# Performance work log

Measured on AMD Instinct MI355X. Metric: run time of the kernel, lower is better.

## Reference

```python
import jax, jax.numpy as jnp
import numpy as np

N_NODES = 100000
D_IN = 128
H_DIM = 128
N_EDGES = 1600000


def _gcn_conv(x, src, dst, dinv, W, b):
    # PyG GCNConv(improved=True): h = x @ W; out = A_hat h + b,
    # A_hat = D^{-1/2} (A + 2I) D^{-1/2}
    h = x @ W                                   # [N, H]
    norm = dinv[src] * dinv[dst]                # [E]
    agg = jnp.zeros_like(h).at[dst].add(h[src] * norm[:, None])
    agg = agg + h * (2.0 * dinv * dinv)[:, None]  # self-loop, weight 2.0
    return agg + b


def setup_inputs() -> dict:
    key = jax.random.key(0)
    ks = jax.random.split(key, 12)
    s = 1.0 / np.sqrt(D_IN)
    sh = 1.0 / np.sqrt(2 * H_DIM)
    inp = {
        "x": jax.random.normal(ks[0], (N_NODES, D_IN), jnp.float32),
        "edge_index": jax.random.randint(ks[1], (2, N_EDGES), 0, N_NODES, jnp.int64),
        # GCNConv weights (in -> hidden), bias
        "Wz": jax.random.uniform(ks[2], (D_IN, H_DIM), jnp.float32, -s, s),
        "bz": jnp.zeros((H_DIM,), jnp.float32),
        "Wr": jax.random.uniform(ks[3], (D_IN, H_DIM), jnp.float32, -s, s),
        "br": jnp.zeros((H_DIM,), jnp.float32),
        "Wh": jax.random.uniform(ks[4], (D_IN, H_DIM), jnp.float32, -s, s),
        "bh": jnp.zeros((H_DIM,), jnp.float32),
        # TGCN gate linears: Linear(2h, h)
        "lzW": jax.random.uniform(ks[5], (2 * H_DIM, H_DIM), jnp.float32, -sh, sh),
        "lzb": jax.random.uniform(ks[6], (H_DIM,), jnp.float32, -sh, sh),
        "lrW": jax.random.uniform(ks[7], (2 * H_DIM, H_DIM), jnp.float32, -sh, sh),
        "lrb": jax.random.uniform(ks[8], (H_DIM,), jnp.float32, -sh, sh),
        "lhW": jax.random.uniform(ks[9], (2 * H_DIM, H_DIM), jnp.float32, -sh, sh),
        "lhb": jax.random.uniform(ks[10], (H_DIM,), jnp.float32, -sh, sh),
        # final linear2: hidden -> 1
        "W2": jax.random.uniform(ks[11], (H_DIM, 1), jnp.float32, -1 / np.sqrt(H_DIM), 1 / np.sqrt(H_DIM)),
        "b2": jnp.zeros((1,), jnp.float32),
    }
    return inp


def reference(x, edge_index, Wz, bz, Wr, br, Wh, bh, lzW, lzb, lrW, lrb, lhW, lhb, W2, b2):
    src, dst = edge_index[0], edge_index[1]
    n = x.shape[0]
    # improved GCN norm: deg includes self-loop weight 2
    deg = jnp.zeros((n,), x.dtype).at[dst].add(jnp.ones_like(src, x.dtype)) + 2.0
    dinv = jnp.where(deg > 0, deg ** -0.5, 0.0)
    # TGCN cell with H0 = 0
    H0 = jnp.zeros((n, Wz.shape[1]), x.dtype)
    Z = jax.nn.sigmoid(jnp.concatenate([_gcn_conv(x, src, dst, dinv, Wz, bz), H0], axis=1) @ lzW + lzb)
    R = jax.nn.sigmoid(jnp.concatenate([_gcn_conv(x, src, dst, dinv, Wr, br), H0], axis=1) @ lrW + lrb)
    Ht = jnp.tanh(jnp.concatenate([_gcn_conv(x, src, dst, dinv, Wh, bh), H0 * R], axis=1) @ lhW + lhb)
    H = Z * H0 + (1.0 - Z) * Ht
    # forward: relu output is discarded (y = h overwrites), then linear2
    return H @ W2 + b2
```

## Files before the change

### kernel.cpp

```cpp
#include <hip/hip_runtime.h>
#include <math.h>

#define D 128
#define BSHIFT 9
#define NB 196
#define EPT 7
#define P1B 241
#define CAPB 80
#define PSTRIDE (P1B * CAPB)
#define ECAP 9216
#define XCB2 3125
#define PRB 32

typedef __attribute__((ext_vector_type(8))) short s8v;
typedef __attribute__((ext_vector_type(8))) unsigned short us8;
typedef __attribute__((ext_vector_type(4))) unsigned short us4;
typedef __attribute__((ext_vector_type(4))) float f4v;

__device__ __forceinline__ float bf2f(unsigned short u) {
    union { unsigned int i; float f; } v; v.i = ((unsigned int)u) << 16; return v.f;
}
__device__ __forceinline__ unsigned short f2bf(float f) {
    union { float f; unsigned int i; } v; v.f = f;
    unsigned int r = v.i + 0x7FFFu + ((v.i >> 16) & 1u);
    return (unsigned short)(r >> 16);
}

__global__ __launch_bounds__(1024) void k_pre(
    const int* __restrict__ src, const int* __restrict__ dst, int E,
    unsigned int* __restrict__ pairs, int* __restrict__ runlen,
    const float* __restrict__ x, unsigned short* __restrict__ xb, int n4,
    const float* __restrict__ Wz, const float* __restrict__ bz,
    const float* __restrict__ lzW, const float* __restrict__ lzb,
    const float* __restrict__ Wh, const float* __restrict__ bh,
    const float* __restrict__ lhW, const float* __restrict__ lhb,
    unsigned short* __restrict__ Mt, float* __restrict__ c) {
    __shared__ int cnt[256];
    __shared__ int loff[256];
    __shared__ unsigned int stage[EPT * 1024];
    int bx = blockIdx.x, tid = threadIdx.x;

    if (bx < P1B) {
        unsigned int pk[EPT]; int rkbk[EPT];
        int e0 = bx * (EPT * 1024) + tid;
        if (tid < 256) cnt[tid] = 0;
        __syncthreads();
        #pragma unroll
        for (int i = 0; i < EPT; ++i) {
            int e = e0 + i * 1024;
            bool ok = e < E;
            int d = ok ? dst[e] : 0;
            int s = ok ? src[e] : 0;
            int bk = d >> BSHIFT;
            pk[i] = ((unsigned int)(d & ((1 << BSHIFT) - 1)) << 17) | (unsigned int)s;
            int r = ok ? atomicAdd(&cnt[bk], 1) : 0;
            rkbk[i] = ok ? ((bk << 16) | r) : -1;
        }
        __syncthreads();
        if (tid < 64) {
            int v0 = cnt[tid * 4], v1 = cnt[tid * 4 + 1], v2 = cnt[tid * 4 + 2], v3 = cnt[tid * 4 + 3];
            int s = v0 + v1 + v2 + v3;
            int sc = s;
            #pragma unroll
            for (int off = 1; off < 64; off <<= 1) {
                int o = __shfl_up(sc, off, 64);
                if (tid >= off) sc += o;
            }
            int excl = sc - s;
            loff[tid * 4]     = excl;
            loff[tid * 4 + 1] = excl + v0;
            loff[tid * 4 + 2] = excl + v0 + v1;
            loff[tid * 4 + 3] = excl + v0 + v1 + v2;
        }
        __syncthreads();
        #pragma unroll
        for (int i = 0; i < EPT; ++i) {
            if (rkbk[i] >= 0) {
                int bk = rkbk[i] >> 16;
                stage[loff[bk] + (rkbk[i] & 0xffff)] = pk[i];
            }
        }
        if (tid < 256) runlen[bx * 256 + tid] = cnt[tid];
        __syncthreads();
        int wv = tid >> 6, lane = tid & 63;
        for (int b = wv; b < 256; b += 16) {
            int len = cnt[b];
            if (len == 0) continue;
            int lo = loff[b];
            unsigned int gbase = (unsigned int)b * PSTRIDE + (unsigned int)bx * CAPB;
            for (int j = lane; j < len; j += 64)
                pairs[gbase + j] = stage[lo + j];
        }
    } else if (bx < P1B + XCB2) {
        int i = (bx - P1B) * 1024 + tid;
        if (i < n4) {
            float4 v = ((const float4*)x)[i];
            us4 o;
            o[0] = f2bf(v.x); o[1] = f2bf(v.y); o[2] = f2bf(v.z); o[3] = f2bf(v.w);
            ((us4*)xb)[i] = o;
        }
    } else {
        int k = (bx - (P1B + XCB2)) * 4 + (tid >> 8);
        int j = tid & 255;
        int jj = j & 127;
        const float* W = (j < 128) ? Wz : Wh;
        const float* L = (j < 128) ? lzW : lhW;
        float s = 0.f;
        for (int t = 0; t < 128; ++t) s += W[k * 128 + t] * L[t * 128 + jj];
        Mt[(size_t)j * 128 + k] = f2bf(s);
        if (k == 0) {
            const float* b  = (j < 128) ? bz  : bh;
            const float* lb = (j < 128) ? lzb : lhb;
            float cs = lb[jj];
            for (int t = 0; t < 128; ++t) cs += b[t] * L[t * 128 + jj];
            c[j] = cs;
        }
    }
}

__global__ __launch_bounds__(1024) void k_part2(
    const unsigned int* __restrict__ pairs, const int* __restrict__ runlen,
    int N,
    int* __restrict__ rowptr, int* __restrict__ deg, float* __restrict__ dinv,
    int* __restrict__ esrc) {
    __shared__ int cnt2[512];
    __shared__ int lcur[512];
    __shared__ int rl[256];
    __shared__ int sstage[ECAP];
    __shared__ int stot;
    int b = blockIdx.x, tid = threadIdx.x;
    int n0 = b << BSHIFT;
    int nn = min(N - n0, 1 << BSHIFT);
    long pb = (long)b * PSTRIDE;
    int wv = tid >> 6, lane = tid & 63;

    if (tid < 256) rl[tid] = (tid < P1B) ? runlen[tid * 256 + b] : 0;
    if (tid < 512) cnt2[tid] = 0;
    __syncthreads();
    for (int r = wv; r < P1B; r += 16) {
        int len = rl[r];
        long rb = pb + r * CAPB;
        for (int j = lane; j < len; j += 64)
            atomicAdd(&cnt2[pairs[rb + j] >> 17], 1);
    }
    __syncthreads();
    if (tid < 64) {
        int v[8]; int s = 0;
        #pragma unroll
        for (int k = 0; k < 8; ++k) { v[k] = cnt2[tid * 8 + k]; s += v[k]; }
        int sc = s;
        #pragma unroll
        for (int off = 1; off < 64; off <<= 1) {
            int o = __shfl_up(sc, off, 64);
            if (tid >= off) sc += o;
        }
        int excl = sc - s;
        if (tid == 63) stot = sc;
        #pragma unroll
        for (int k = 0; k < 8; ++k) {
            int node = tid * 8 + k;
            lcur[node] = excl;
            if (node < nn) {
                rowptr[n0 + node] = b * ECAP + excl;
                deg[n0 + node]    = v[k];
                dinv[n0 + node]   = rsqrtf((float)v[k] + 2.0f);
            }
            excl += v[k];
        }
    }
    __syncthreads();
    for (int r = wv; r < P1B; r += 16) {
        int len = rl[r];
        long rb = pb + r * CAPB;
        for (int j = lane; j < len; j += 64) {
            unsigned int p = pairs[rb + j];
            int pos = atomicAdd(&lcur[p >> 17], 1);
            sstage[pos] = (int)(p & 0x1FFFFu);
        }
    }
    __syncthreads();
    int tot = stot;
    for (int i = tid; i < tot; i += 1024)
        esrc[b * ECAP + i] = sstage[i];
}

#define ASTRIDE 136
__global__ __launch_bounds__(512, 6) void k_gep(
    const unsigned short* __restrict__ xb,
    const int* __restrict__ esrc, const int* __restrict__ rowptr,
    const int* __restrict__ deg, const float* __restrict__ dinv,
    const unsigned short* __restrict__ Mt, const float* __restrict__ c,
    const float* __restrict__ W2, const float* __restrict__ b2,
    float* __restrict__ out, int N) {
    __shared__ unsigned short Ast[32 * ASTRIDE];
    __shared__ float pbuf[8][32];

    int tid = threadIdx.x;
    int n0 = blockIdx.x * 32;
    int grp = tid >> 4, sub = tid & 15;
    int node = n0 + grp;
    bool valid = node < N;

    int start = 0, dcnt = 0;
    float dd = 0.f;
    us8 xs = {0, 0, 0, 0, 0, 0, 0, 0};
    if (valid) {
        start = rowptr[node];
        dcnt  = deg[node];
        dd    = dinv[node];
        xs = *(const us8*)(xb + (size_t)node * D + sub * 8);
    }
    float acc[8];
    #pragma unroll
    for (int j = 0; j < 8; ++j) acc[j] = 0.f;

    for (int base = 0; base < dcnt; base += 16) {
        int cnt = min(16, dcnt - base);
        int myedge = 0; float mynorm = 0.f;
        if (sub < cnt) { myedge = esrc[start + base + sub]; mynorm = dinv[myedge]; }
        int i = 0;
        for (; i + 3 < cnt; i += 4) {
            int   s0 = __shfl(myedge, i,     16); float w0 = __shfl(mynorm, i,     16);
            int   s1 = __shfl(myedge, i + 1, 16); float w1 = __shfl(mynorm, i + 1, 16);
            int   s2 = __shfl(myedge, i + 2, 16); float w2 = __shfl(mynorm, i + 2, 16);
            int   s3 = __shfl(myedge, i + 3, 16); float w3 = __shfl(mynorm, i + 3, 16);
            us8 v0 = *(const us8*)(xb + (size_t)s0 * D + sub * 8);
            us8 v1 = *(const us8*)(xb + (size_t)s1 * D + sub * 8);
            us8 v2 = *(const us8*)(xb + (size_t)s2 * D + sub * 8);
            us8 v3 = *(const us8*)(xb + (size_t)s3 * D + sub * 8);
            #pragma unroll
            for (int j = 0; j < 8; ++j) acc[j] += bf2f(v0[j]) * w0;
            #pragma unroll
            for (int j = 0; j < 8; ++j) acc[j] += bf2f(v1[j]) * w1;
            #pragma unroll
            for (int j = 0; j < 8; ++j) acc[j] += bf2f(v2[j]) * w2;
            #pragma unroll
            for (int j = 0; j < 8; ++j) acc[j] += bf2f(v3[j]) * w3;
        }
        for (; i < cnt; ++i) {
            int   s0 = __shfl(myedge, i, 16); float w0 = __shfl(mynorm, i, 16);
            us8 v0 = *(const us8*)(xb + (size_t)s0 * D + sub * 8);
            #pragma unroll
            for (int j = 0; j < 8; ++j) acc[j] += bf2f(v0[j]) * w0;
        }
    }
    {
        float sfac = 2.f * dd * dd;
        us8 r;
        #pragma unroll
        for (int j = 0; j < 8; ++j) r[j] = f2bf(acc[j] * dd + bf2f(xs[j]) * sfac);
        *(us8*)&Ast[grp * ASTRIDE + sub * 8] = r;
    }
    __syncthreads();

    int wv = tid >> 6;
    int lane = tid & 63;
    int l = lane & 15, q = lane >> 4;

    f4v acc2[2][2];
    #pragma unroll
    for (int zi = 0; zi < 2; ++zi)
        #pragma unroll
        for (int nt = 0; nt < 2; ++nt) acc2[zi][nt] = (f4v){0.f, 0.f, 0.f, 0.f};

    const unsigned short* Bb = Mt + (size_t)l * 128 + q * 8;

    #pragma unroll
    for (int ks = 0; ks < 4; ++ks) {
        s8v bz_ = *(const s8v*)(Bb + (size_t)wv * 16 * 128 + ks * 32);
        s8v bh_ = *(const s8v*)(Bb + (size_t)(8 + wv) * 16 * 128 + ks * 32);
        #pragma unroll
        for (int nt = 0; nt < 2; ++nt) {
            s8v a = *(const s8v*)&Ast[(nt * 16 + l) * ASTRIDE + ks * 32 + q * 8];
            acc2[0][nt] = __builtin_amdgcn_mfma_f32_16x16x32_bf16(a, bz_, acc2[0][nt], 0, 0, 0);
            acc2[1][nt] = __builtin_amdgcn_mfma_f32_16x16x32_bf16(a, bh_, acc2[1][nt], 0, 0, 0);
        }
    }

    {
        int col = wv * 16 + l;
        float cz = c[col], ch = c[128 + col], w2 = W2[col];
        float p[2][4];
        #pragma unroll
        for (int nt = 0; nt < 2; ++nt)
            #pragma unroll
            for (int r = 0; r < 4; ++r) {
                float gz = acc2[0][nt][r] + cz;
                float gh = acc2[1][nt][r] + ch;
                float z  = 1.f / (1.f + __expf(-gz));
                float ht = 1.f - 2.f / (__expf(2.f * gh) + 1.f);
                p[nt][r] = (1.f - z) * ht * w2;
            }
        #pragma unroll
        for (int nt = 0; nt < 2; ++nt)
            #pragma unroll
            for (int r = 0; r < 4; ++r) {
                p[nt][r] += __shfl_xor(p[nt][r], 1);
                p[nt][r] += __shfl_xor(p[nt][r], 2);
                p[nt][r] += __shfl_xor(p[nt][r], 4);
                p[nt][r] += __shfl_xor(p[nt][r], 8);
            }
        if (l == 0) {
            #pragma unroll
            for (int nt = 0; nt < 2; ++nt)
                #pragma unroll
                for (int r = 0; r < 4; ++r)
                    pbuf[wv][nt * 16 + q * 4 + r] = p[nt][r];
        }
    }
    __syncthreads();
    if (tid < 32) {
        int n = n0 + tid;
        if (n < N) {
            float s = b2[0];
            #pragma unroll
            for (int cp = 0; cp < 8; ++cp) s += pbuf[cp][tid];
            out[n] = s;
        }
    }
}

extern "C" void kernel_launch(void* const* d_in, const int* in_sizes, int n_in,
                              void* d_out, int out_size, void* d_ws, size_t ws_size,
                              hipStream_t stream) {
    const float* x    = (const float*)d_in[0];
    const int*   eidx = (const int*)d_in[1];
    const float* Wz   = (const float*)d_in[2];
    const float* bz   = (const float*)d_in[3];
    const float* Wh   = (const float*)d_in[6];
    const float* bh   = (const float*)d_in[7];
    const float* lzW  = (const float*)d_in[8];
    const float* lzb  = (const float*)d_in[9];
    const float* lhW  = (const float*)d_in[12];
    const float* lhb  = (const float*)d_in[13];
    const float* W2   = (const float*)d_in[14];
    const float* b2   = (const float*)d_in[15];
    float* out = (float*)d_out;

    int N = in_sizes[0] / D;
    int E = in_sizes[1] / 2;
    const int* src = eidx;
    const int* dst = eidx + E;

    char* ws = (char*)d_ws;
    size_t off = 0;
    auto alloc = [&](size_t bytes) { void* p = ws + off; off += (bytes + 511) & ~(size_t)511; return p; };
    unsigned short* xb  = (unsigned short*)alloc((size_t)N * D * 2);
    unsigned int*   pairs = (unsigned int*)alloc((size_t)NB * PSTRIDE * 4);
    int*   rowptr = (int*)  alloc((size_t)N * 4);
    int*   deg    = (int*)  alloc((size_t)N * 4);
    float* dinv   = (float*)alloc((size_t)N * 4);
    int*   esrc   = (int*)  alloc((size_t)NB * ECAP * 4);
    int*   runlen = (int*)  alloc((size_t)P1B * 256 * 4);
    unsigned short* Mt = (unsigned short*)alloc(256 * 128 * 2);
    float* c      = (float*)alloc(256 * 4);

    int n4 = N * (D / 4);
    k_pre<<<P1B + XCB2 + PRB, 1024, 0, stream>>>(
        src, dst, E, pairs, runlen,
        x, xb, n4, Wz, bz, lzW, lzb, Wh, bh, lhW, lhb, Mt, c);
    k_part2<<<NB, 1024, 0, stream>>>(pairs, runlen, N, rowptr, deg, dinv, esrc);
    k_gep<<<(N + 31) / 32, 512, 0, stream>>>(
        xb, esrc, rowptr, deg, dinv, Mt, c, W2, b2, out, N);
}
```

Before: 231.2 us.

## Process 64 nodes per gather block with split-edge half-warps and coarsen bf16 cast

The gather-GEMM kernel now handles 64 nodes per block. Each 32-lane group processes four node rows in sequence, and its two 16-lane halves take alternating edges, then combine partial sums with a shuffle-xor. The MFMA stage now covers four 16-row tiles per wave, so each loaded B fragment from Mt is reused across more rows. The x-to-bf16 conversion blocks each process four float4 chunks per thread, giving fewer blocks. This aims to amortize per-block overhead and Mt loads and to raise memory-level parallelism in the gather. The cost is fewer blocks, more LDS use and higher register pressure.

```diff
diff --git a/kernel.cpp b/kernel.cpp
--- a/kernel.cpp
+++ b/kernel.cpp
@@ -9,7 +9,7 @@
 #define CAPB 80
 #define PSTRIDE (P1B * CAPB)
 #define ECAP 9216
-#define XCB2 3125
+#define XCB4 782
 #define PRB 32
 
 typedef __attribute__((ext_vector_type(8))) short s8v;
@@ -91,16 +91,20 @@
             for (int j = lane; j < len; j += 64)
                 pairs[gbase + j] = stage[lo + j];
         }
-    } else if (bx < P1B + XCB2) {
-        int i = (bx - P1B) * 1024 + tid;
-        if (i < n4) {
-            float4 v = ((const float4*)x)[i];
-            us4 o;
-            o[0] = f2bf(v.x); o[1] = f2bf(v.y); o[2] = f2bf(v.z); o[3] = f2bf(v.w);
-            ((us4*)xb)[i] = o;
+    } else if (bx < P1B + XCB4) {
+        int i0 = (bx - P1B) * 4096 + tid;
+        #pragma unroll
+        for (int u = 0; u < 4; ++u) {
+            int i = i0 + u * 1024;
+            if (i < n4) {
+                float4 v = ((const float4*)x)[i];
+                us4 o;
+                o[0] = f2bf(v.x); o[1] = f2bf(v.y); o[2] = f2bf(v.z); o[3] = f2bf(v.w);
+                ((us4*)xb)[i] = o;
+            }
         }
     } else {
-        int k = (bx - (P1B + XCB2)) * 4 + (tid >> 8);
+        int k = (bx - (P1B + XCB4)) * 4 + (tid >> 8);
         int j = tid & 255;
         int jj = j & 127;
         const float* W = (j < 128) ? Wz : Wh;
@@ -192,64 +196,74 @@
     const unsigned short* __restrict__ Mt, const float* __restrict__ c,
     const float* __restrict__ W2, const float* __restrict__ b2,
     float* __restrict__ out, int N) {
-    __shared__ unsigned short Ast[32 * ASTRIDE];
-    __shared__ float pbuf[8][32];
+    __shared__ unsigned short Ast[64 * ASTRIDE];
+    __shared__ float pbuf[8][64];
 
     int tid = threadIdx.x;
-    int n0 = blockIdx.x * 32;
-    int grp = tid >> 4, sub = tid & 15;
-    int node = n0 + grp;
-    bool valid = node < N;
-
-    int start = 0, dcnt = 0;
-    float dd = 0.f;
-    us8 xs = {0, 0, 0, 0, 0, 0, 0, 0};
-    if (valid) {
-        start = rowptr[node];
-        dcnt  = deg[node];
-        dd    = dinv[node];
-        xs = *(const us8*)(xb + (size_t)node * D + sub * 8);
-    }
-    float acc[8];
-    #pragma unroll
-    for (int j = 0; j < 8; ++j) acc[j] = 0.f;
-
-    for (int base = 0; base < dcnt; base += 16) {
-        int cnt = min(16, dcnt - base);
-        int myedge = 0; float mynorm = 0.f;
-        if (sub < cnt) { myedge = esrc[start + base + sub]; mynorm = dinv[myedge]; }
-        int i = 0;
-        for (; i + 3 < cnt; i += 4) {
-            int   s0 = __shfl(myedge, i,     16); float w0 = __shfl(mynorm, i,     16);
-            int   s1 = __shfl(myedge, i + 1, 16); float w1 = __shfl(mynorm, i + 1, 16);
-            int   s2 = __shfl(myedge, i + 2, 16); float w2 = __shfl(mynorm, i + 2, 16);
-            int   s3 = __shfl(myedge, i + 3, 16); float w3 = __shfl(mynorm, i + 3, 16);
-            us8 v0 = *(const us8*)(xb + (size_t)s0 * D + sub * 8);
-            us8 v1 = *(const us8*)(xb + (size_t)s1 * D + sub * 8);
-            us8 v2 = *(const us8*)(xb + (size_t)s2 * D + sub * 8);
-            us8 v3 = *(const us8*)(xb + (size_t)s3 * D + sub * 8);
-            #pragma unroll
-            for (int j = 0; j < 8; ++j) acc[j] += bf2f(v0[j]) * w0;
-            #pragma unroll
-            for (int j = 0; j < 8; ++j) acc[j] += bf2f(v1[j]) * w1;
-            #pragma unroll
-            for (int j = 0; j < 8; ++j) acc[j] += bf2f(v2[j]) * w2;
-            #pragma unroll
-            for (int j = 0; j < 8; ++j) acc[j] += bf2f(v3[j]) * w3;
-        }
-        for (; i < cnt; ++i) {
-            int   s0 = __shfl(myedge, i, 16); float w0 = __shfl(mynorm, i, 16);
-            us8 v0 = *(const us8*)(xb + (size_t)s0 * D + sub * 8);
-            #pragma unroll
-            for (int j = 0; j < 8; ++j) acc[j] += bf2f(v0[j]) * w0;
-        }
-    }
-    {
-        float sfac = 2.f * dd * dd;
-        us8 r;
-        #pragma unroll
-        for (int j = 0; j < 8; ++j) r[j] = f2bf(acc[j] * dd + bf2f(xs[j]) * sfac);
-        *(us8*)&Ast[grp * ASTRIDE + sub * 8] = r;
+    int n0 = blockIdx.x * 64;
+    int hw = tid >> 5, sub = tid & 31;
+    int eo = sub >> 4, cs = sub & 15;
+
+    for (int t = 0; t < 4; ++t) {
+        int row = t * 16 + hw;
+        int node = n0 + row;
+        bool valid = node < N;
+        int start = 0, dcnt = 0;
+        float dd = 0.f;
+        us8 xs = {0, 0, 0, 0, 0, 0, 0, 0};
+        if (valid) {
+            start = rowptr[node];
+            dcnt  = deg[node];
+            dd    = dinv[node];
+            if (eo == 0) xs = *(const us8*)(xb + (size_t)node * D + cs * 8);
+        }
+        float acc[8];
+        #pragma unroll
+        for (int j = 0; j < 8; ++j) acc[j] = 0.f;
+
+        int end = start + dcnt;
+        for (int base = start; base < end; base += 32) {
+            int cnt = min(32, end - base);
+            int myedge = 0; float mynorm = 0.f;
+            if (sub < cnt) { myedge = esrc[base + sub]; mynorm = dinv[myedge]; }
+            int npairs = (cnt + 1) >> 1;
+            int i = 0;
+            for (; i + 3 < npairs; i += 4) {
+                int i0 = 2 * i + eo;
+                int   s0 = __shfl(myedge, i0,     32); float w0 = __shfl(mynorm, i0,     32);
+                int   s1 = __shfl(myedge, i0 + 2, 32); float w1 = __shfl(mynorm, i0 + 2, 32);
+                int   s2 = __shfl(myedge, i0 + 4, 32); float w2 = __shfl(mynorm, i0 + 4, 32);
+                int   s3 = __shfl(myedge, i0 + 6, 32); float w3 = __shfl(mynorm, i0 + 6, 32);
+                us8 v0 = *(const us8*)(xb + (size_t)s0 * D + cs * 8);
+                us8 v1 = *(const us8*)(xb + (size_t)s1 * D + cs * 8);
+                us8 v2 = *(const us8*)(xb + (size_t)s2 * D + cs * 8);
+                us8 v3 = *(const us8*)(xb + (size_t)s3 * D + cs * 8);
+                #pragma unroll
+                for (int j = 0; j < 8; ++j) acc[j] += bf2f(v0[j]) * w0;
+                #pragma unroll
+                for (int j = 0; j < 8; ++j) acc[j] += bf2f(v1[j]) * w1;
+                #pragma unroll
+                for (int j = 0; j < 8; ++j) acc[j] += bf2f(v2[j]) * w2;
+                #pragma unroll
+                for (int j = 0; j < 8; ++j) acc[j] += bf2f(v3[j]) * w3;
+            }
+            for (; i < npairs; ++i) {
+                int i0 = 2 * i + eo;
+                int   s0 = __shfl(myedge, i0, 32); float w0 = __shfl(mynorm, i0, 32);
+                us8 v0 = *(const us8*)(xb + (size_t)s0 * D + cs * 8);
+                #pragma unroll
+                for (int j = 0; j < 8; ++j) acc[j] += bf2f(v0[j]) * w0;
+            }
+        }
+        #pragma unroll
+        for (int j = 0; j < 8; ++j) acc[j] += __shfl_xor(acc[j], 16);
+        if (eo == 0) {
+            float sfac = 2.f * dd * dd;
+            us8 r;
+            #pragma unroll
+            for (int j = 0; j < 8; ++j) r[j] = f2bf(acc[j] * dd + bf2f(xs[j]) * sfac);
+            *(us8*)&Ast[row * ASTRIDE + cs * 8] = r;
+        }
     }
     __syncthreads();
 
@@ -257,11 +271,11 @@
     int lane = tid & 63;
     int l = lane & 15, q = lane >> 4;
 
-    f4v acc2[2][2];
+    f4v acc2[2][4];
     #pragma unroll
     for (int zi = 0; zi < 2; ++zi)
         #pragma unroll
-        for (int nt = 0; nt < 2; ++nt) acc2[zi][nt] = (f4v){0.f, 0.f, 0.f, 0.f};
+        for (int nt = 0; nt < 4; ++nt) acc2[zi][nt] = (f4v){0.f, 0.f, 0.f, 0.f};
 
     const unsigned short* Bb = Mt + (size_t)l * 128 + q * 8;
 
@@ -270,7 +284,7 @@
         s8v bz_ = *(const s8v*)(Bb + (size_t)wv * 16 * 128 + ks * 32);
         s8v bh_ = *(const s8v*)(Bb + (size_t)(8 + wv) * 16 * 128 + ks * 32);
         #pragma unroll
-        for (int nt = 0; nt < 2; ++nt) {
+        for (int nt = 0; nt < 4; ++nt) {
             s8v a = *(const s8v*)&Ast[(nt * 16 + l) * ASTRIDE + ks * 32 + q * 8];
             acc2[0][nt] = __builtin_amdgcn_mfma_f32_16x16x32_bf16(a, bz_, acc2[0][nt], 0, 0, 0);
             acc2[1][nt] = __builtin_amdgcn_mfma_f32_16x16x32_bf16(a, bh_, acc2[1][nt], 0, 0, 0);
@@ -280,9 +294,9 @@
     {
         int col = wv * 16 + l;
         float cz = c[col], ch = c[128 + col], w2 = W2[col];
-        float p[2][4];
-        #pragma unroll
-        for (int nt = 0; nt < 2; ++nt)
+        float p[4][4];
+        #pragma unroll
+        for (int nt = 0; nt < 4; ++nt)
             #pragma unroll
             for (int r = 0; r < 4; ++r) {
                 float gz = acc2[0][nt][r] + cz;
@@ -292,7 +306,7 @@
                 p[nt][r] = (1.f - z) * ht * w2;
             }
         #pragma unroll
-        for (int nt = 0; nt < 2; ++nt)
+        for (int nt = 0; nt < 4; ++nt)
             #pragma unroll
             for (int r = 0; r < 4; ++r) {
                 p[nt][r] += __shfl_xor(p[nt][r], 1);
@@ -302,14 +316,14 @@
             }
         if (l == 0) {
             #pragma unroll
-            for (int nt = 0; nt < 2; ++nt)
+            for (int nt = 0; nt < 4; ++nt)
                 #pragma unroll
                 for (int r = 0; r < 4; ++r)
                     pbuf[wv][nt * 16 + q * 4 + r] = p[nt][r];
         }
     }
     __syncthreads();
-    if (tid < 32) {
+    if (tid < 64) {
         int n = n0 + tid;
         if (n < N) {
             float s = b2[0];
@@ -356,10 +370,10 @@
     float* c      = (float*)alloc(256 * 4);
 
     int n4 = N * (D / 4);
-    k_pre<<<P1B + XCB2 + PRB, 1024, 0, stream>>>(
+    k_pre<<<P1B + XCB4 + PRB, 1024, 0, stream>>>(
         src, dst, E, pairs, runlen,
         x, xb, n4, Wz, bz, lzW, lzb, Wh, bh, lhW, lhb, Mt, c);
     k_part2<<<NB, 1024, 0, stream>>>(pairs, runlen, N, rowptr, deg, dinv, esrc);
-    k_gep<<<(N + 31) / 32, 512, 0, stream>>>(
+    k_gep<<<(N + 63) / 64, 512, 0, stream>>>(
         xb, esrc, rowptr, deg, dinv, Mt, c, W2, b2, out, N);
 }
```

New measurement: 235.2 us. No clear change (+1.7%).
